# Performance work log

Measured on AMD Instinct MI355X. Metric: run time of the kernel, lower is better.

Reference implementation:

```python
import jax, jax.numpy as jnp
import numpy as np

HIGH, LOW = 768, 384
LOW2 = LOW // 2  # PNL uses low_dim // reduc_ratio, reduc_ratio=2
B, N = 8, 4096
EPS = 1e-5


def _nl_block(x_h, x_l, wg, bg, wt, bt, wp, bp, ww, bw, gamma, beta):
    # x_h: [B,N,H], x_l: [B,N0,H]; conv1x1 == per-token linear
    Nl = x_l.shape[1]
    g = jnp.einsum('bnc,dc->bnd', x_l, wg) + bg      # [B,N0,D]
    th = jnp.einsum('bnc,dc->bnd', x_h, wt) + bt     # [B,N,D]
    ph = jnp.einsum('bnc,dc->bnd', x_l, wp) + bp     # [B,N0,D]
    # attention = (th @ ph^T) / N0; y = attention @ g. Reassociate:
    kv = jnp.einsum('bnd,bne->bde', ph, g) / Nl      # [B,D,D]
    y = jnp.einsum('bnd,bde->bne', th, kv)           # [B,N,D]
    y = jnp.einsum('bnd,cd->bnc', y, ww) + bw        # [B,N,H]
    # BatchNorm1d over channel dim, training-mode batch stats (biased var)
    mu = y.mean(axis=(0, 1))
    var = y.var(axis=(0, 1))
    y = (y - mu) * jax.lax.rsqrt(var + EPS) * gamma + beta
    return y + x_h


def setup_inputs() -> dict:
    key = jax.random.key(0)
    ks = jax.random.split(key, 24)
    s = 0.02
    d = {
        'x': jax.random.normal(ks[0], (B, N, HIGH), jnp.float32),
        'x0': jax.random.normal(ks[1], (B, N, HIGH), jnp.float32),
        # CNL params (low_dim = 384)
        'c_wg': s * jax.random.normal(ks[2], (LOW, HIGH)), 'c_bg': s * jax.random.normal(ks[3], (LOW,)),
        'c_wt': s * jax.random.normal(ks[4], (LOW, HIGH)), 'c_bt': s * jax.random.normal(ks[5], (LOW,)),
        'c_wp': s * jax.random.normal(ks[6], (LOW, HIGH)), 'c_bp': s * jax.random.normal(ks[7], (LOW,)),
        'c_ww': s * jax.random.normal(ks[8], (HIGH, LOW)), 'c_bw': s * jax.random.normal(ks[9], (HIGH,)),
        'c_gamma': 1.0 + 0.1 * jax.random.normal(ks[10], (HIGH,)),
        'c_beta': s * jax.random.normal(ks[11], (HIGH,)),
        # PNL params (low_dim // 2 = 192)
        'p_wg': s * jax.random.normal(ks[12], (LOW2, HIGH)), 'p_bg': s * jax.random.normal(ks[13], (LOW2,)),
        'p_wt': s * jax.random.normal(ks[14], (LOW2, HIGH)), 'p_bt': s * jax.random.normal(ks[15], (LOW2,)),
        'p_wp': s * jax.random.normal(ks[16], (LOW2, HIGH)), 'p_bp': s * jax.random.normal(ks[17], (LOW2,)),
        'p_ww': s * jax.random.normal(ks[18], (HIGH, LOW2)), 'p_bw': s * jax.random.normal(ks[19], (HIGH,)),
        'p_gamma': 1.0 + 0.1 * jax.random.normal(ks[20], (HIGH,)),
        'p_beta': s * jax.random.normal(ks[21], (HIGH,)),
    }
    return d


def reference(x, x0,
              c_wg, c_bg, c_wt, c_bt, c_wp, c_bp, c_ww, c_bw, c_gamma, c_beta,
              p_wg, p_bg, p_wt, p_bt, p_wp, p_bp, p_ww, p_bw, p_gamma, p_beta):
    z = _nl_block(x, x0, c_wg, c_bg, c_wt, c_bt, c_wp, c_bp, c_ww, c_bw, c_gamma, c_beta)
    out = _nl_block(z, x0, p_wg, p_bg, p_wt, p_bt, p_wp, p_bp, p_ww, p_bw, p_gamma, p_beta)
    return out
```

## Files before the change

### kernel.cpp

```cpp
#include <hip/hip_runtime.h>
#include <stdint.h>

typedef unsigned short u16;
typedef __bf16 bf16x8 __attribute__((ext_vector_type(8)));
typedef short s16x8 __attribute__((ext_vector_type(8)));
typedef short s16x4 __attribute__((ext_vector_type(4)));
typedef float f32x4 __attribute__((ext_vector_type(4)));

__device__ __forceinline__ u16 f2bf(float f) {
  uint32_t u = __builtin_bit_cast(uint32_t, f);
  u += 0x7fffu + ((u >> 16) & 1u);
  return (u16)(u >> 16);
}
__device__ __forceinline__ float bf2f(u16 h) {
  uint32_t u = ((uint32_t)h) << 16;
  return __builtin_bit_cast(float, u);
}

__device__ __forceinline__ void gl16(const u16* g, u16* l) {
  __builtin_amdgcn_global_load_lds(
      (const __attribute__((address_space(1))) void*)g,
      (__attribute__((address_space(3))) void*)l, 16, 0, 0);
}

__global__ void cvt_in2(const float* __restrict__ a, const float* __restrict__ b,
                        u16* __restrict__ da, u16* __restrict__ db, long n8each) {
  long stride = (long)gridDim.x * blockDim.x;
  long total = 2 * n8each;
  for (long i = (long)blockIdx.x * blockDim.x + threadIdx.x; i < total; i += stride) {
    const float* src = (i < n8each) ? a + i * 8 : b + (i - n8each) * 8;
    u16* dst = (i < n8each) ? da + i * 8 : db + (i - n8each) * 8;
    const f32x4* s = (const f32x4*)src;
    f32x4 v0 = s[0], v1 = s[1];
    s16x8 o;
#pragma unroll
    for (int j = 0; j < 4; ++j) o[j] = (short)f2bf(v0[j]);
#pragma unroll
    for (int j = 0; j < 4; ++j) o[4 + j] = (short)f2bf(v1[j]);
    *(s16x8*)dst = o;
  }
}

__global__ void cvt_flat8(const float* __restrict__ src, u16* __restrict__ dst,
                          long n8, float scale) {
  long stride = (long)gridDim.x * blockDim.x;
  for (long i = (long)blockIdx.x * blockDim.x + threadIdx.x; i < n8; i += stride) {
    const f32x4* s = (const f32x4*)(src + i * 8);
    f32x4 a = s[0], b = s[1];
    s16x8 o;
#pragma unroll
    for (int j = 0; j < 4; ++j) o[j] = (short)f2bf(a[j] * scale);
#pragma unroll
    for (int j = 0; j < 4; ++j) o[4 + j] = (short)f2bf(b[j] * scale);
    *(s16x8*)(dst + i * 8) = o;
  }
}

__global__ void prep_w(const float* __restrict__ c_wg, const float* __restrict__ c_wp,
                       const float* __restrict__ p_wg, const float* __restrict__ p_wp,
                       const float* __restrict__ c_wt, const float* __restrict__ p_wt,
                       const float* __restrict__ c_ww, const float* __restrict__ p_ww,
                       u16* __restrict__ wcat, u16* __restrict__ wt_c,
                       u16* __restrict__ wt_p, u16* __restrict__ ww_c,
                       u16* __restrict__ ww_p) {
  const int C0 = 1280 * 768 / 4;
  const int C1 = C0 + 384 * 768 / 4;
  const int C2 = C1 + 256 * 768 / 4;
  const int C3 = C2 + 768 * 384 / 4;
  const int C4 = C3 + 768 * 256 / 4;
  int stride = gridDim.x * blockDim.x;
  for (int i = blockIdx.x * blockDim.x + threadIdx.x; i < C4; i += stride) {
    const float* src = nullptr;
    u16* dst;
    if (i < C0) {
      int e = i * 4;
      dst = wcat + e;
      int r = e / 768;
      if (r < 384) src = c_wg + e;
      else if (r < 768) src = c_wp + e - 384 * 768;
      else if (r < 960) src = p_wg + e - 768 * 768;
      else if (r < 1024) src = nullptr;
      else if (r < 1216) src = p_wp + e - 1024 * 768;
      else src = nullptr;
    } else if (i < C1) {
      int e = (i - C0) * 4; dst = wt_c + e; src = c_wt + e;
    } else if (i < C2) {
      int e = (i - C1) * 4; dst = wt_p + e;
      src = (e / 768 < 192) ? p_wt + e : nullptr;
    } else if (i < C3) {
      int e = (i - C2) * 4; dst = ww_c + e; src = c_ww + e;
    } else {
      int e = (i - C3) * 4; dst = ww_p + e;
      int r = e >> 8, c = e & 255;
      src = (c < 192) ? p_ww + r * 192 + c : nullptr;
    }
    s16x4 o;
    if (src) {
      f32x4 v = *(const f32x4*)src;
#pragma unroll
      for (int j = 0; j < 4; ++j) o[j] = (short)f2bf(v[j]);
    } else {
      o = s16x4{0, 0, 0, 0};
    }
    *(s16x4*)dst = o;
  }
}

__global__ void prep_b(const float* __restrict__ c_bg, const float* __restrict__ c_bp,
                       const float* __restrict__ p_bg, const float* __restrict__ p_bp,
                       const float* __restrict__ c_bt, const float* __restrict__ p_bt,
                       float* __restrict__ biasb, float* __restrict__ sums) {
  int i = blockIdx.x * blockDim.x + threadIdx.x;
  if (i < 1920) {
    float v = 0.f;
    if (i < 384) v = c_bg[i];
    else if (i < 768) v = c_bp[i - 384];
    else if (i < 960) v = p_bg[i - 768];
    else if (i < 1024) v = 0.f;
    else if (i < 1216) v = p_bp[i - 1024];
    else if (i < 1280) v = 0.f;
    else if (i < 1664) v = c_bt[i - 1280];
    else if (i < 1856) v = p_bt[i - 1664];
    biasb[i] = v;
  } else if (i < 1920 + 3072) {
    sums[i - 1920] = 0.f;
  }
}

template <int BIAS, int OUT_ATOMIC, int SUMS>
__global__ __launch_bounds__(256) void gemm_nt(
    const u16* __restrict__ A, const u16* __restrict__ B, void* __restrict__ Cv,
    const float* __restrict__ bias, float* __restrict__ sums,
    int ntiles, long lda, long ldb, long ldc, int K,
    long aBatch, long bBatch, long cBatch) {
  __shared__ u16 As[2][128 * 32];
  __shared__ u16 Bs[2][128 * 32];

  const int bm = blockIdx.x / ntiles;
  const int bn = blockIdx.x % ntiles;
  const int bb = blockIdx.y;
  const int kChunk = K / gridDim.z;
  const long k0base = (long)blockIdx.z * kChunk;
  const int nt = kChunk >> 5;

  const u16* Ab = A + (long)bb * aBatch + (long)bm * 128 * lda + k0base;
  const u16* Bb = B + (long)bb * bBatch + (long)bn * 128 * ldb + k0base;

  const int t = threadIdx.x;
  const int w = t >> 6;
  const int l = t & 63;
  const int wr = w >> 1, wc = w & 1;

  const long aoff = (long)(32 * w + (l >> 2)) * lda + (l & 3) * 8;
  const long boff = (long)(32 * w + (l >> 2)) * ldb + (l & 3) * 8;

  f32x4 acc[4][4] = {};

  gl16(Ab + aoff, &As[0][(32 * w) * 32]);
  gl16(Ab + aoff + 16 * lda, &As[0][(32 * w + 16) * 32]);
  gl16(Bb + boff, &Bs[0][(32 * w) * 32]);
  gl16(Bb + boff + 16 * ldb, &Bs[0][(32 * w + 16) * 32]);
  if (nt > 1) {
    gl16(Ab + aoff + 32, &As[1][(32 * w) * 32]);
    gl16(Ab + aoff + 16 * lda + 32, &As[1][(32 * w + 16) * 32]);
    gl16(Bb + boff + 32, &Bs[1][(32 * w) * 32]);
    gl16(Bb + boff + 16 * ldb + 32, &Bs[1][(32 * w + 16) * 32]);
  }

  for (int tt = 0; tt < nt; ++tt) {
    const int cur = tt & 1;
    if (tt + 1 < nt)
      asm volatile("s_waitcnt vmcnt(4)" ::: "memory");
    else
      asm volatile("s_waitcnt vmcnt(0)" ::: "memory");
    __builtin_amdgcn_s_barrier();

    const int kq = (l >> 4) * 8;
    bf16x8 af[4], bfr[4];
#pragma unroll
    for (int mi = 0; mi < 4; ++mi)
      af[mi] = __builtin_bit_cast(
          bf16x8, *(const s16x8*)(&As[cur][(wr * 64 + mi * 16 + (l & 15)) * 32 + kq]));
#pragma unroll
    for (int ni = 0; ni < 4; ++ni)
      bfr[ni] = __builtin_bit_cast(
          bf16x8, *(const s16x8*)(&Bs[cur][(wc * 64 + ni * 16 + (l & 15)) * 32 + kq]));
#pragma unroll
    for (int mi = 0; mi < 4; ++mi)
#pragma unroll
      for (int ni = 0; ni < 4; ++ni)
        acc[mi][ni] = __builtin_amdgcn_mfma_f32_16x16x32_bf16(
            af[mi], bfr[ni], acc[mi][ni], 0, 0, 0);

    __builtin_amdgcn_s_barrier();
    if (tt + 2 < nt) {
      const long ko = (long)(tt + 2) * 32;
      gl16(Ab + aoff + ko, &As[cur][(32 * w) * 32]);
      gl16(Ab + aoff + 16 * lda + ko, &As[cur][(32 * w + 16) * 32]);
      gl16(Bb + boff + ko, &Bs[cur][(32 * w) * 32]);
      gl16(Bb + boff + 16 * ldb + ko, &Bs[cur][(32 * w + 16) * 32]);
    }
  }
  __builtin_amdgcn_sched_barrier(0);

  const long crow0 = (long)bm * 128 + wr * 64;
  const long ccol0 = (long)bn * 128 + wc * 64;

  if (OUT_ATOMIC) {
    float* C = (float*)Cv + (long)bb * cBatch;
#pragma unroll
    for (int mi = 0; mi < 4; ++mi)
#pragma unroll
      for (int j = 0; j < 4; ++j) {
        long row = crow0 + mi * 16 + (l >> 4) * 4 + j;
#pragma unroll
        for (int ni = 0; ni < 4; ++ni) {
          long col = ccol0 + ni * 16 + (l & 15);
          atomicAdd(&C[row * ldc + col], acc[mi][ni][j]);
        }
      }
  } else {
    u16* C = (u16*)Cv + (long)bb * cBatch;
#pragma unroll
    for (int mi = 0; mi < 4; ++mi)
#pragma unroll
      for (int j = 0; j < 4; ++j) {
        long row = crow0 + mi * 16 + (l >> 4) * 4 + j;
        float rb = (BIAS == 1) ? bias[row] : 0.f;
#pragma unroll
        for (int ni = 0; ni < 4; ++ni) {
          long col = ccol0 + ni * 16 + (l & 15);
          float cb = (BIAS == 2) ? bias[col] : 0.f;
          C[row * ldc + col] = f2bf(acc[mi][ni][j] + rb + cb);
        }
      }
  }

  if (SUMS) {
#pragma unroll
    for (int ni = 0; ni < 4; ++ni) {
      float s = 0.f, q = 0.f;
#pragma unroll
      for (int mi = 0; mi < 4; ++mi)
#pragma unroll
        for (int j = 0; j < 4; ++j) {
          float v = acc[mi][ni][j];
          s += v;
          q += v * v;
        }
      s += __shfl_xor(s, 16);
      q += __shfl_xor(q, 16);
      s += __shfl_xor(s, 32);
      q += __shfl_xor(q, 32);
      if (l < 16) {
        long col = ccol0 + ni * 16 + l;
        atomicAdd(&sums[col], s);
        atomicAdd(&sums[768 + col], q);
      }
    }
  }
}

__global__ void bn_stats(const float* __restrict__ sums, const float* __restrict__ gamma,
                         const float* __restrict__ beta, float* __restrict__ stats,
                         float invN) {
  int c = threadIdx.x;
  float mu = sums[c] * invN;
  float var = sums[768 + c] * invN - mu * mu;
  float sc = gamma[c] * rsqrtf(var + 1e-5f);
  stats[c] = sc;
  stats[768 + c] = beta[c] - mu * sc;
}

template <int OUT_F32>
__global__ void bn_apply(const u16* __restrict__ pre, const u16* __restrict__ resid,
                         const float* __restrict__ stats, void* __restrict__ out,
                         long n8) {
  long stride = (long)gridDim.x * blockDim.x;
  for (long i = (long)blockIdx.x * blockDim.x + threadIdx.x; i < n8; i += stride) {
    long base = i * 8;
    int c = (int)(base % 768);
    f32x4 sc0 = *(const f32x4*)(stats + c);
    f32x4 sc1 = *(const f32x4*)(stats + c + 4);
    f32x4 sh0 = *(const f32x4*)(stats + 768 + c);
    f32x4 sh1 = *(const f32x4*)(stats + 768 + c + 4);
    s16x8 p = *(const s16x8*)(pre + base);
    s16x8 rv = *(const s16x8*)(resid + base);
    float o[8];
#pragma unroll
    for (int j = 0; j < 4; ++j)
      o[j] = bf2f((u16)p[j]) * sc0[j] + sh0[j] + bf2f((u16)rv[j]);
#pragma unroll
    for (int j = 0; j < 4; ++j)
      o[4 + j] = bf2f((u16)p[4 + j]) * sc1[j] + sh1[j] + bf2f((u16)rv[4 + j]);
    if (OUT_F32) {
      f32x4 o0, o1;
#pragma unroll
      for (int j = 0; j < 4; ++j) { o0[j] = o[j]; o1[j] = o[4 + j]; }
      f32x4* op = (f32x4*)((float*)out + base);
      op[0] = o0;
      op[1] = o1;
    } else {
      s16x8 ov;
#pragma unroll
      for (int j = 0; j < 8; ++j) ov[j] = (short)f2bf(o[j]);
      *(s16x8*)((u16*)out + base) = ov;
    }
  }
}

extern "C" void kernel_launch(void* const* d_in, const int* in_sizes, int n_in,
                              void* d_out, int out_size, void* d_ws, size_t ws_size,
                              hipStream_t stream) {
  const float* x = (const float*)d_in[0];
  const float* x0 = (const float*)d_in[1];
  const float* c_wg = (const float*)d_in[2];
  const float* c_bg = (const float*)d_in[3];
  const float* c_wt = (const float*)d_in[4];
  const float* c_bt = (const float*)d_in[5];
  const float* c_wp = (const float*)d_in[6];
  const float* c_bp = (const float*)d_in[7];
  const float* c_ww = (const float*)d_in[8];
  const float* c_gamma = (const float*)d_in[10];
  const float* c_beta = (const float*)d_in[11];
  const float* p_wg = (const float*)d_in[12];
  const float* p_bg = (const float*)d_in[13];
  const float* p_wt = (const float*)d_in[14];
  const float* p_bt = (const float*)d_in[15];
  const float* p_wp = (const float*)d_in[16];
  const float* p_bp = (const float*)d_in[17];
  const float* p_ww = (const float*)d_in[18];
  const float* p_gamma = (const float*)d_in[20];
  const float* p_beta = (const float*)d_in[21];

  char* ws = (char*)d_ws;
  const long NT = 32768;
  u16* xbf = (u16*)(ws + 0);
  u16* x0bf = (u16*)(ws + 50331648);
  u16* th = (u16*)(ws + 50331648);
  float* kvf_c = (float*)(ws + 75497472);
  float* kvf_p = (float*)(ws + 80216064);
  u16* kvb = (u16*)(ws + 82313216);
  u16* kvwT = (u16*)(ws + 84672512);
  u16* gphT = (u16*)(ws + 100663296);
  u16* wcat = (u16*)(ws + 184549376);
  u16* wt_c = (u16*)(ws + 186515456);
  u16* wt_p = (u16*)(ws + 187105280);
  u16* ww_c = (u16*)(ws + 187498496);
  u16* ww_p = (u16*)(ws + 188088320);
  float* biasb = (float*)(ws + 188481536);
  float* sums = (float*)(ws + 188489216);
  float* stats = (float*)(ws + 188501504);
  u16* zbf = xbf;
  u16* pre = gphT;

  cvt_in2<<<4096, 256, 0, stream>>>(x, x0, xbf, x0bf, NT * 768 / 8);
  prep_w<<<480, 256, 0, stream>>>(c_wg, c_wp, p_wg, p_wp, c_wt, p_wt, c_ww, p_ww,
                                  wcat, wt_c, wt_p, ww_c, ww_p);
  prep_b<<<20, 256, 0, stream>>>(c_bg, c_bp, p_bg, p_bp, c_bt, p_bt, biasb, sums);

  gemm_nt<1, 0, 0><<<dim3(10 * 256, 1, 1), 256, 0, stream>>>(
      wcat, x0bf, gphT, biasb, nullptr, 256, 768, 768, 32768, 768, 0, 0, 0);
  hipMemsetAsync(kvf_c, 0, 4718592 + 2097152, stream);

  gemm_nt<2, 0, 0><<<dim3(256 * 3, 1, 1), 256, 0, stream>>>(
      xbf, wt_c, th, biasb + 1280, nullptr, 3, 768, 768, 384, 768, 0, 0, 0);
  gemm_nt<0, 1, 0><<<dim3(9, 8, 8), 256, 0, stream>>>(
      gphT + (long)384 * 32768, gphT, kvf_c, nullptr, nullptr, 3, 32768, 32768,
      384, 4096, 4096, 4096, (long)384 * 384);
  cvt_flat8<<<576, 256, 0, stream>>>(kvf_c, kvb, (long)8 * 384 * 384 / 8, 1.f / 4096.f);
  gemm_nt<0, 0, 0><<<dim3(18, 8, 1), 256, 0, stream>>>(
      ww_c, kvb, kvwT, nullptr, nullptr, 3, 384, 384, 384, 384, 0,
      (long)384 * 384, (long)768 * 384);
  gemm_nt<0, 0, 1><<<dim3(192, 8, 1), 256, 0, stream>>>(
      th, kvwT, pre, nullptr, sums, 6, 384, 384, 768, 384, (long)4096 * 384,
      (long)768 * 384, (long)4096 * 768);
  bn_stats<<<1, 768, 0, stream>>>(sums, c_gamma, c_beta, stats, 1.f / 32768.f);
  bn_apply<0><<<2048, 256, 0, stream>>>(pre, xbf, stats, zbf, NT * 768 / 8);

  gemm_nt<2, 0, 0><<<dim3(256 * 2, 1, 1), 256, 0, stream>>>(
      zbf, wt_p, th, biasb + 1664, nullptr, 2, 768, 768, 256, 768, 0, 0, 0);
  gemm_nt<0, 1, 0><<<dim3(4, 8, 8), 256, 0, stream>>>(
      gphT + (long)1024 * 32768, gphT + (long)768 * 32768, kvf_p, nullptr, nullptr,
      2, 32768, 32768, 256, 4096, 4096, 4096, (long)256 * 256);
  cvt_flat8<<<256, 256, 0, stream>>>(kvf_p, kvb, (long)8 * 256 * 256 / 8, 1.f / 4096.f);
  gemm_nt<0, 0, 0><<<dim3(12, 8, 1), 256, 0, stream>>>(
      ww_p, kvb, kvwT, nullptr, nullptr, 2, 256, 256, 256, 256, 0,
      (long)256 * 256, (long)768 * 256);
  gemm_nt<0, 0, 1><<<dim3(192, 8, 1), 256, 0, stream>>>(
      th, kvwT, pre, nullptr, sums + 1536, 6, 256, 256, 768, 256, (long)4096 * 256,
      (long)768 * 256, (long)4096 * 768);
  bn_stats<<<1, 768, 0, stream>>>(sums + 1536, p_gamma, p_beta, stats, 1.f / 32768.f);
  bn_apply<1><<<2048, 256, 0, stream>>>(pre, zbf, stats, (float*)d_out, NT * 768 / 8);
}
```

Baseline: 452.8 us.

## Add 256x256-tile 512-thread GEMM with 4-stage prefetch for large projections

Introduces a new GEMM kernel using 256x256 output tiles, 8 waves, and a 4-deep LDS ring buffer. It interleaves global-to-LDS prefetch with two half-tile MFMA phases and raises wave priority around the MFMA blocks. The kernel is used for the fused g/phi projection and both y·Wᵀ output GEMMs, where the larger tile gives more reuse per byte loaded. The trade-offs are 128 KB of LDS per block and fewer blocks (e.g. 384 for the output GEMMs), which can leave CUs underused.

```diff
diff --git a/kernel.cpp b/kernel.cpp
--- a/kernel.cpp
+++ b/kernel.cpp
@@ -21,6 +21,10 @@
   __builtin_amdgcn_global_load_lds(
       (const __attribute__((address_space(1))) void*)g,
       (__attribute__((address_space(3))) void*)l, 16, 0, 0);
+}
+
+__device__ __forceinline__ void barf() {
+  asm volatile("s_barrier" ::: "memory");
 }
 
 __global__ void cvt_in2(const float* __restrict__ a, const float* __restrict__ b,
@@ -127,6 +131,147 @@
   }
 }
 
+template <int BIAS, int SUMS>
+__global__ __launch_bounds__(512) void gemm_nt_big(
+    const u16* __restrict__ A, const u16* __restrict__ B, void* __restrict__ Cv,
+    const float* __restrict__ bias, float* __restrict__ sums,
+    int ntiles, long lda, long ldb, long ldc, int K,
+    long aBatch, long bBatch, long cBatch) {
+  __shared__ u16 As[4][256 * 32];
+  __shared__ u16 Bs[4][256 * 32];
+
+  const int bm = blockIdx.x / ntiles;
+  const int bn = blockIdx.x % ntiles;
+  const int bb = blockIdx.y;
+  const int nt = K >> 5;
+
+  const u16* Ab = A + (long)bb * aBatch + (long)bm * 256 * lda;
+  const u16* Bb = B + (long)bb * bBatch + (long)bn * 256 * ldb;
+
+  const int t = threadIdx.x;
+  const int w = t >> 6;
+  const int l = t & 63;
+  const int wr = w >> 2;
+  const int wc = w & 3;
+
+  const int srow = w * 16 + (l >> 2);
+  const long aoff0 = (long)srow * lda + (l & 3) * 8;
+  const long aoff1 = (long)(128 + srow) * lda + (l & 3) * 8;
+  const long boff0 = (long)srow * ldb + (l & 3) * 8;
+  const long boff1 = (long)(128 + srow) * ldb + (l & 3) * 8;
+
+#define STAGE_A(T, BUF)                                   \
+  gl16(Ab + aoff0 + (long)(T) * 32, &As[BUF][w * 512]);   \
+  gl16(Ab + aoff1 + (long)(T) * 32, &As[BUF][(8 + w) * 512]);
+#define STAGE_B(T, BUF)                                   \
+  gl16(Bb + boff0 + (long)(T) * 32, &Bs[BUF][w * 512]);   \
+  gl16(Bb + boff1 + (long)(T) * 32, &Bs[BUF][(8 + w) * 512]);
+
+  f32x4 acc[8][4] = {};
+
+  STAGE_A(0, 0); STAGE_B(0, 0);
+  if (nt > 1) { STAGE_A(1, 1); STAGE_B(1, 1); }
+  if (nt > 2) { STAGE_A(2, 2); STAGE_B(2, 2); }
+  if (nt > 2)      asm volatile("s_waitcnt vmcnt(8)" ::: "memory");
+  else if (nt > 1) asm volatile("s_waitcnt vmcnt(4)" ::: "memory");
+  else             asm volatile("s_waitcnt vmcnt(0)" ::: "memory");
+  barf();
+
+  const int kq = (l >> 4) * 8;
+  const int ar = wr * 128 + (l & 15);
+  const int br = wc * 64 + (l & 15);
+
+  for (int tt = 0; tt < nt; ++tt) {
+    const int cur = tt & 3;
+    const int pf = (tt + 3) & 3;
+    const bool do_pf = (tt + 3) < nt;
+
+    bf16x8 bfr[4], af[4];
+#pragma unroll
+    for (int ni = 0; ni < 4; ++ni)
+      bfr[ni] = __builtin_bit_cast(
+          bf16x8, *(const s16x8*)(&Bs[cur][(br + ni * 16) * 32 + kq]));
+#pragma unroll
+    for (int mi = 0; mi < 4; ++mi)
+      af[mi] = __builtin_bit_cast(
+          bf16x8, *(const s16x8*)(&As[cur][(ar + mi * 16) * 32 + kq]));
+    if (do_pf) { STAGE_A(tt + 3, pf); }
+    barf();
+    __builtin_amdgcn_s_setprio(1);
+#pragma unroll
+    for (int mi = 0; mi < 4; ++mi)
+#pragma unroll
+      for (int ni = 0; ni < 4; ++ni)
+        acc[mi][ni] = __builtin_amdgcn_mfma_f32_16x16x32_bf16(
+            af[mi], bfr[ni], acc[mi][ni], 0, 0, 0);
+    __builtin_amdgcn_s_setprio(0);
+    barf();
+
+    bf16x8 ag[4];
+#pragma unroll
+    for (int mi = 0; mi < 4; ++mi)
+      ag[mi] = __builtin_bit_cast(
+          bf16x8, *(const s16x8*)(&As[cur][(ar + 64 + mi * 16) * 32 + kq]));
+    if (do_pf) { STAGE_B(tt + 3, pf); }
+    barf();
+    __builtin_amdgcn_s_setprio(1);
+#pragma unroll
+    for (int mi = 0; mi < 4; ++mi)
+#pragma unroll
+      for (int ni = 0; ni < 4; ++ni)
+        acc[4 + mi][ni] = __builtin_amdgcn_mfma_f32_16x16x32_bf16(
+            ag[mi], bfr[ni], acc[4 + mi][ni], 0, 0, 0);
+    __builtin_amdgcn_s_setprio(0);
+    if (tt + 4 <= nt)      asm volatile("s_waitcnt vmcnt(8)" ::: "memory");
+    else if (tt + 3 == nt) asm volatile("s_waitcnt vmcnt(4)" ::: "memory");
+    else if (tt + 2 == nt) asm volatile("s_waitcnt vmcnt(0)" ::: "memory");
+    barf();
+  }
+#undef STAGE_A
+#undef STAGE_B
+  __builtin_amdgcn_sched_barrier(0);
+
+  const long crow0 = (long)bm * 256 + wr * 128;
+  const long ccol0 = (long)bn * 256 + wc * 64;
+  u16* C = (u16*)Cv + (long)bb * cBatch;
+#pragma unroll
+  for (int mi = 0; mi < 8; ++mi)
+#pragma unroll
+    for (int j = 0; j < 4; ++j) {
+      long row = crow0 + mi * 16 + (l >> 4) * 4 + j;
+      float rb = (BIAS == 1) ? bias[row] : 0.f;
+#pragma unroll
+      for (int ni = 0; ni < 4; ++ni) {
+        long col = ccol0 + ni * 16 + (l & 15);
+        C[row * ldc + col] = f2bf(acc[mi][ni][j] + rb);
+      }
+    }
+
+  if (SUMS) {
+#pragma unroll
+    for (int ni = 0; ni < 4; ++ni) {
+      float s = 0.f, q = 0.f;
+#pragma unroll
+      for (int mi = 0; mi < 8; ++mi)
+#pragma unroll
+        for (int j = 0; j < 4; ++j) {
+          float v = acc[mi][ni][j];
+          s += v;
+          q += v * v;
+        }
+      s += __shfl_xor(s, 16);
+      q += __shfl_xor(q, 16);
+      s += __shfl_xor(s, 32);
+      q += __shfl_xor(q, 32);
+      if (l < 16) {
+        long col = ccol0 + ni * 16 + l;
+        atomicAdd(&sums[col], s);
+        atomicAdd(&sums[768 + col], q);
+      }
+    }
+  }
+}
+
 template <int BIAS, int OUT_ATOMIC, int SUMS>
 __global__ __launch_bounds__(256) void gemm_nt(
     const u16* __restrict__ A, const u16* __restrict__ B, void* __restrict__ Cv,
@@ -359,8 +504,8 @@
                                   wcat, wt_c, wt_p, ww_c, ww_p);
   prep_b<<<20, 256, 0, stream>>>(c_bg, c_bp, p_bg, p_bp, c_bt, p_bt, biasb, sums);
 
-  gemm_nt<1, 0, 0><<<dim3(10 * 256, 1, 1), 256, 0, stream>>>(
-      wcat, x0bf, gphT, biasb, nullptr, 256, 768, 768, 32768, 768, 0, 0, 0);
+  gemm_nt_big<1, 0><<<dim3(5 * 128, 1, 1), 512, 0, stream>>>(
+      wcat, x0bf, gphT, biasb, nullptr, 128, 768, 768, 32768, 768, 0, 0, 0);
   hipMemsetAsync(kvf_c, 0, 4718592 + 2097152, stream);
 
   gemm_nt<2, 0, 0><<<dim3(256 * 3, 1, 1), 256, 0, stream>>>(
@@ -372,8 +517,8 @@
   gemm_nt<0, 0, 0><<<dim3(18, 8, 1), 256, 0, stream>>>(
       ww_c, kvb, kvwT, nullptr, nullptr, 3, 384, 384, 384, 384, 0,
       (long)384 * 384, (long)768 * 384);
-  gemm_nt<0, 0, 1><<<dim3(192, 8, 1), 256, 0, stream>>>(
-      th, kvwT, pre, nullptr, sums, 6, 384, 384, 768, 384, (long)4096 * 384,
+  gemm_nt_big<0, 1><<<dim3(48, 8, 1), 512, 0, stream>>>(
+      th, kvwT, pre, nullptr, sums, 3, 384, 384, 768, 384, (long)4096 * 384,
       (long)768 * 384, (long)4096 * 768);
   bn_stats<<<1, 768, 0, stream>>>(sums, c_gamma, c_beta, stats, 1.f / 32768.f);
   bn_apply<0><<<2048, 256, 0, stream>>>(pre, xbf, stats, zbf, NT * 768 / 8);
@@ -387,8 +532,8 @@
   gemm_nt<0, 0, 0><<<dim3(12, 8, 1), 256, 0, stream>>>(
       ww_p, kvb, kvwT, nullptr, nullptr, 2, 256, 256, 256, 256, 0,
       (long)256 * 256, (long)768 * 256);
-  gemm_nt<0, 0, 1><<<dim3(192, 8, 1), 256, 0, stream>>>(
-      th, kvwT, pre, nullptr, sums + 1536, 6, 256, 256, 768, 256, (long)4096 * 256,
+  gemm_nt_big<0, 1><<<dim3(48, 8, 1), 512, 0, stream>>>(
+      th, kvwT, pre, nullptr, sums + 1536, 3, 256, 256, 768, 256, (long)4096 * 256,
       (long)768 * 256, (long)4096 * 768);
   bn_stats<<<1, 768, 0, stream>>>(sums + 1536, p_gamma, p_beta, stats, 1.f / 32768.f);
   bn_apply<1><<<2048, 256, 0, stream>>>(pre, zbf, stats, (float*)d_out, NT * 768 / 8);
```

New measurement: 458.1 us. No clear change (+1.2%).
